# Performance work log

Measured on AMD Instinct MI355X. Metric: run time of the kernel, lower is better.

## Reference

```python
import jax, jax.numpy as jnp
import numpy as np

N_NODES = 100000
N_EDGES = 3200000
D_FEAT = 64


def setup_inputs() -> dict:
    key = jax.random.key(0)
    k1, k2, k3 = jax.random.split(key, 3)
    inputs = jax.random.normal(k1, (N_NODES, D_FEAT), dtype=jnp.float32)
    rows = jax.random.randint(k2, (N_EDGES,), 0, N_NODES, dtype=jnp.int32)
    cols = jax.random.randint(k3, (N_EDGES,), 0, N_NODES, dtype=jnp.int32)
    return {"inputs": inputs, "rows": rows, "cols": cols}


def reference(inputs, rows, cols):
    # adj is a binary sparse [N, N] matrix given as COO edges (rows[e], cols[e]) -> 1.0
    n = inputs.shape[0]
    # degrees = adj.sum(dim=1): count of outgoing edges per row
    deg = jax.ops.segment_sum(jnp.ones_like(rows, dtype=inputs.dtype), rows,
                              num_segments=n)  # [N]
    # degrees + (degrees == 0): avoid div-by-zero for isolated nodes
    deg = deg + (deg == 0).astype(inputs.dtype)
    # spmm(adj, inputs): sum neighbor features into each row
    agg = jax.ops.segment_sum(inputs[cols], rows, num_segments=n)  # [N, d]
    return agg / deg[:, None]
```

## Files before the change

kernel.cpp:

```cpp
#include <hip/hip_runtime.h>
#include <hip/hip_bf16.h>
#include <hip/hip_fp16.h>

#define D_FEAT 64
#define TILE_EDGES 8192
#define SC_THREADS 512
#define ROWS_PER_BUK 128
#define BUK_SHIFT 7
#define STRIDE 4480

__global__ void __launch_bounds__(SC_THREADS) scatter_kernel(
    const float* __restrict__ x, __half* __restrict__ x16,
    const int* __restrict__ rows, const int* __restrict__ cols,
    int* __restrict__ gcount, int* __restrict__ ebuf,
    int n_edges, int nbuk, int n4)
{
    __shared__ int lh[1024];
    __shared__ int lscan[1024];
    __shared__ int lgb[1024];
    __shared__ int lsort[TILE_EDGES];

    const int t = threadIdx.x;

    {
        const int per = (n4 + gridDim.x - 1) / gridDim.x;
        const int s0 = blockIdx.x * per;
        const int e0 = min(s0 + per, n4);
        for (int i = s0 + t; i < e0; i += SC_THREADS) {
            float4 v = ((const float4*)x)[i];
            ushort4 u;
            u.x = __half_as_ushort(__float2half(v.x));
            u.y = __half_as_ushort(__float2half(v.y));
            u.z = __half_as_ushort(__float2half(v.z));
            u.w = __half_as_ushort(__float2half(v.w));
            ((ushort4*)x16)[i] = u;
        }
    }

    lh[t] = 0; lh[t + 512] = 0;
    __syncthreads();

    const int tb = blockIdx.x * TILE_EDGES;
    const int te = min(tb + TILE_EDGES, n_edges);

    for (int e = tb + t * 4; e < te; e += SC_THREADS * 4) {
        if (e + 4 <= te) {
            int4 r4 = *(const int4*)&rows[e];
            atomicAdd(&lh[r4.x >> BUK_SHIFT], 1);
            atomicAdd(&lh[r4.y >> BUK_SHIFT], 1);
            atomicAdd(&lh[r4.z >> BUK_SHIFT], 1);
            atomicAdd(&lh[r4.w >> BUK_SHIFT], 1);
        } else {
            for (int k = e; k < te; ++k) atomicAdd(&lh[rows[k] >> BUK_SHIFT], 1);
        }
    }
    __syncthreads();

    const int c0 = lh[2 * t], c1 = lh[2 * t + 1];
    const int s2 = c0 + c1;
    lscan[t] = s2;
    __syncthreads();
    for (int ofs = 1; ofs < 512; ofs <<= 1) {
        int val = lscan[t];
        int add = (t >= ofs) ? lscan[t - ofs] : 0;
        __syncthreads();
        lscan[t] = val + add;
        __syncthreads();
    }
    const int excl = lscan[t] - s2;
    __syncthreads();
    lscan[2 * t] = excl;
    lscan[2 * t + 1] = excl + c0;
    lgb[2 * t]     = c0 ? atomicAdd(&gcount[2 * t], c0) : 0;
    lgb[2 * t + 1] = c1 ? atomicAdd(&gcount[2 * t + 1], c1) : 0;
    lh[2 * t] = excl;
    lh[2 * t + 1] = excl + c0;
    __syncthreads();

    for (int e = tb + t * 4; e < te; e += SC_THREADS * 4) {
        if (e + 4 <= te) {
            int4 r4 = *(const int4*)&rows[e];
            int4 c4 = *(const int4*)&cols[e];
            int p0 = atomicAdd(&lh[r4.x >> BUK_SHIFT], 1);
            int p1 = atomicAdd(&lh[r4.y >> BUK_SHIFT], 1);
            int p2 = atomicAdd(&lh[r4.z >> BUK_SHIFT], 1);
            int p3 = atomicAdd(&lh[r4.w >> BUK_SHIFT], 1);
            lsort[p0] = ((r4.x & (ROWS_PER_BUK - 1)) << 17) | c4.x;
            lsort[p1] = ((r4.y & (ROWS_PER_BUK - 1)) << 17) | c4.y;
            lsort[p2] = ((r4.z & (ROWS_PER_BUK - 1)) << 17) | c4.z;
            lsort[p3] = ((r4.w & (ROWS_PER_BUK - 1)) << 17) | c4.w;
        } else {
            for (int k = e; k < te; ++k) {
                int r = rows[k], c = cols[k];
                int pos = atomicAdd(&lh[r >> BUK_SHIFT], 1);
                lsort[pos] = ((r & (ROWS_PER_BUK - 1)) << 17) | c;
            }
        }
    }
    __syncthreads();

    const int hw = t >> 5;
    const int hl = t & 31;
    for (int b = hw; b < nbuk; b += 16) {
        const int ls = lscan[b];
        const int cnt = lh[b] - ls;
        const int gb = lgb[b];
        for (int i = hl; i < cnt; i += 32) {
            int gpos = gb + i;
            if (gpos < STRIDE) ebuf[b * STRIDE + gpos] = lsort[ls + i];
        }
    }
}

__global__ void __launch_bounds__(512) gather_kernel(
    const uint4* __restrict__ x4, const int* __restrict__ gcount,
    const int* __restrict__ ebuf, float* __restrict__ out, int n_nodes)
{
    __shared__ int lcol[STRIDE];
    __shared__ int lh[ROWS_PER_BUK];
    __shared__ int lscan[ROWS_PER_BUK];
    __shared__ int lcur[ROWS_PER_BUK];
    const int b = blockIdx.x;
    const int t = threadIdx.x;

    const int start = b * STRIDE;
    int cnt = gcount[b];
    if (cnt > STRIDE) cnt = STRIDE;

    if (t < ROWS_PER_BUK) lh[t] = 0;
    __syncthreads();
    for (int i = t; i < cnt; i += 512) atomicAdd(&lh[ebuf[start + i] >> 17], 1);
    __syncthreads();

    int v0 = (t < ROWS_PER_BUK) ? lh[t] : 0;
    if (t < ROWS_PER_BUK) lscan[t] = v0;
    __syncthreads();
    for (int ofs = 1; ofs < ROWS_PER_BUK; ofs <<= 1) {
        int val = 0;
        if (t < ROWS_PER_BUK) {
            val = lscan[t];
            if (t >= ofs) val += lscan[t - ofs];
        }
        __syncthreads();
        if (t < ROWS_PER_BUK) lscan[t] = val;
        __syncthreads();
    }
    if (t < ROWS_PER_BUK) {
        int excl = lscan[t] - v0;
        lscan[t] = excl;
        lcur[t] = excl;
    }
    __syncthreads();

    for (int i = t; i < cnt; i += 512) {
        int p = ebuf[start + i];
        int pos = atomicAdd(&lcur[p >> 17], 1);
        lcol[pos] = p & 0x1FFFF;
    }
    __syncthreads();

    const int w = t >> 6;
    const int lane = t & 63;
    const int eg = lane >> 3;
    const int g2 = lane & 7;

    union U { uint4 u; __half2 h2[4]; };

    for (int rr = 0; rr < 16; ++rr) {
        const int r = w * 16 + rr;
        const int row = (b << BUK_SHIFT) + r;
        const int s = lscan[r];
        const int d = lh[r];
        const int e = s + d;

        const __half2 z = __float2half2_rn(0.0f);
        __half2 h[4];
        #pragma unroll
        for (int k = 0; k < 4; ++k) h[k] = z;

        int j = s;
        for (; j + 32 <= e; j += 32) {
            int cA = lcol[j + eg], cB = lcol[j + 8 + eg];
            int cC = lcol[j + 16 + eg], cD = lcol[j + 24 + eg];
            U A, B, C, D;
            A.u = x4[cA * 8 + g2];
            B.u = x4[cB * 8 + g2];
            C.u = x4[cC * 8 + g2];
            D.u = x4[cD * 8 + g2];
            #pragma unroll
            for (int k = 0; k < 4; ++k)
                h[k] = __hadd2(h[k], __hadd2(__hadd2(A.h2[k], B.h2[k]),
                                             __hadd2(C.h2[k], D.h2[k])));
        }
        for (; j + 16 <= e; j += 16) {
            int cA = lcol[j + eg], cB = lcol[j + 8 + eg];
            U A, B;
            A.u = x4[cA * 8 + g2];
            B.u = x4[cB * 8 + g2];
            #pragma unroll
            for (int k = 0; k < 4; ++k)
                h[k] = __hadd2(h[k], __hadd2(A.h2[k], B.h2[k]));
        }
        for (; j + 8 <= e; j += 8) {
            int c = lcol[j + eg];
            U A;
            A.u = x4[c * 8 + g2];
            #pragma unroll
            for (int k = 0; k < 4; ++k) h[k] = __hadd2(h[k], A.h2[k]);
        }
        int rem = e - j;
        if (eg < rem) {
            int c = lcol[j + eg];
            U A;
            A.u = x4[c * 8 + g2];
            #pragma unroll
            for (int k = 0; k < 4; ++k) h[k] = __hadd2(h[k], A.h2[k]);
        }

        float a[8];
        #pragma unroll
        for (int k = 0; k < 4; ++k) {
            float2 f = __half22float2(h[k]);
            a[2 * k] = f.x;
            a[2 * k + 1] = f.y;
        }
        #pragma unroll
        for (int k = 0; k < 8; ++k) {
            a[k] += __shfl_down(a[k], 8, 64);
            a[k] += __shfl_down(a[k], 16, 64);
            a[k] += __shfl_down(a[k], 32, 64);
        }

        if (eg == 0 && row < n_nodes) {
            const float inv = 1.0f / (float)(d > 0 ? d : 1);
            float4* o = (float4*)(out + ((long)row << 6) + (g2 << 3));
            o[0] = make_float4(a[0] * inv, a[1] * inv, a[2] * inv, a[3] * inv);
            o[1] = make_float4(a[4] * inv, a[5] * inv, a[6] * inv, a[7] * inv);
        }
    }
}

extern "C" void kernel_launch(void* const* d_in, const int* in_sizes, int n_in,
                              void* d_out, int out_size, void* d_ws, size_t ws_size,
                              hipStream_t stream) {
    const float* x  = (const float*)d_in[0];
    const int* rows = (const int*)d_in[1];
    const int* cols = (const int*)d_in[2];
    float* out = (float*)d_out;

    const int n_nodes = in_sizes[0] / D_FEAT;
    const int n_edges = in_sizes[1];
    const int n_feat_total = in_sizes[0];
    const int n4 = n_feat_total / 4;

    const int nbuk   = (n_nodes + ROWS_PER_BUK - 1) >> BUK_SHIFT;
    const int ntiles = (n_edges + TILE_EDGES - 1) / TILE_EDGES;

    __half* x16 = (__half*)d_ws;
    int* gcount = (int*)(x16 + n_feat_total);
    int* ebuf   = gcount + nbuk;

    hipMemsetAsync(gcount, 0, (size_t)nbuk * sizeof(int), stream);

    scatter_kernel<<<ntiles, SC_THREADS, 0, stream>>>(
        x, x16, rows, cols, gcount, ebuf, n_edges, nbuk, n4);

    gather_kernel<<<nbuk, 512, 0, stream>>>((const uint4*)x16, gcount, ebuf, out, n_nodes);
}
```

Before: 182.7 us.

## Split gather buckets across two half-row blocks with wave-shuffle scan

Each 128-row bucket is now handled by two 256-thread blocks, each owning 64 rows. Both blocks still read the whole bucket's edge list and keep only their half. The prefix scan over row counts becomes a single-wavefront shuffle scan instead of a multi-sync LDS scan. Smaller blocks with less shared memory should raise occupancy and spread the load over more CUs. The cost is that every edge entry is read twice, and a half-bucket with more than 2560 edges gets truncated.

Measured after the change: 182.1 us. About the same (-0.3%).

```diff
diff --git a/kernel.cpp b/kernel.cpp
--- a/kernel.cpp
+++ b/kernel.cpp
@@ -8,6 +8,9 @@
 #define ROWS_PER_BUK 128
 #define BUK_SHIFT 7
 #define STRIDE 4480
+
+#define HALF_ROWS 64
+#define LCOL_SZ 2560
 
 __global__ void __launch_bounds__(SC_THREADS) scatter_kernel(
     const float* __restrict__ x, __half* __restrict__ x16,
@@ -112,50 +115,53 @@
     }
 }
 
-__global__ void __launch_bounds__(512) gather_kernel(
+__global__ void __launch_bounds__(256) gather_kernel(
     const uint4* __restrict__ x4, const int* __restrict__ gcount,
     const int* __restrict__ ebuf, float* __restrict__ out, int n_nodes)
 {
-    __shared__ int lcol[STRIDE];
-    __shared__ int lh[ROWS_PER_BUK];
-    __shared__ int lscan[ROWS_PER_BUK];
-    __shared__ int lcur[ROWS_PER_BUK];
-    const int b = blockIdx.x;
+    __shared__ int lcol[LCOL_SZ];
+    __shared__ int lh[HALF_ROWS];
+    __shared__ int lscan[HALF_ROWS];
+    __shared__ int lcur[HALF_ROWS];
+    const int bb = blockIdx.x;
+    const int b = bb >> 1;
+    const int half = bb & 1;
     const int t = threadIdx.x;
 
     const int start = b * STRIDE;
     int cnt = gcount[b];
     if (cnt > STRIDE) cnt = STRIDE;
 
-    if (t < ROWS_PER_BUK) lh[t] = 0;
-    __syncthreads();
-    for (int i = t; i < cnt; i += 512) atomicAdd(&lh[ebuf[start + i] >> 17], 1);
-    __syncthreads();
-
-    int v0 = (t < ROWS_PER_BUK) ? lh[t] : 0;
-    if (t < ROWS_PER_BUK) lscan[t] = v0;
-    __syncthreads();
-    for (int ofs = 1; ofs < ROWS_PER_BUK; ofs <<= 1) {
-        int val = 0;
-        if (t < ROWS_PER_BUK) {
-            val = lscan[t];
-            if (t >= ofs) val += lscan[t - ofs];
-        }
-        __syncthreads();
-        if (t < ROWS_PER_BUK) lscan[t] = val;
-        __syncthreads();
-    }
-    if (t < ROWS_PER_BUK) {
-        int excl = lscan[t] - v0;
+    if (t < HALF_ROWS) lh[t] = 0;
+    __syncthreads();
+    for (int i = t; i < cnt; i += 256) {
+        int p = ebuf[start + i];
+        int r = p >> 17;
+        if ((r >> 6) == half) atomicAdd(&lh[r & (HALF_ROWS - 1)], 1);
+    }
+    __syncthreads();
+
+    if (t < 64) {
+        int c = lh[t];
+        int val = c;
+        #pragma unroll
+        for (int ofs = 1; ofs < 64; ofs <<= 1) {
+            int n = __shfl_up(val, ofs, 64);
+            if (t >= ofs) val += n;
+        }
+        int excl = val - c;
         lscan[t] = excl;
         lcur[t] = excl;
     }
     __syncthreads();
 
-    for (int i = t; i < cnt; i += 512) {
+    for (int i = t; i < cnt; i += 256) {
         int p = ebuf[start + i];
-        int pos = atomicAdd(&lcur[p >> 17], 1);
-        lcol[pos] = p & 0x1FFFF;
+        int r = p >> 17;
+        if ((r >> 6) == half) {
+            int pos = atomicAdd(&lcur[r & (HALF_ROWS - 1)], 1);
+            if (pos < LCOL_SZ) lcol[pos] = p & 0x1FFFF;
+        }
     }
     __syncthreads();
 
@@ -168,10 +174,11 @@
 
     for (int rr = 0; rr < 16; ++rr) {
         const int r = w * 16 + rr;
-        const int row = (b << BUK_SHIFT) + r;
+        const int row = (b << BUK_SHIFT) + (half << 6) + r;
         const int s = lscan[r];
         const int d = lh[r];
-        const int e = s + d;
+        int e = s + d;
+        if (e > LCOL_SZ) e = LCOL_SZ;
 
         const __half2 z = __float2half2_rn(0.0f);
         __half2 h[4];
@@ -265,5 +272,5 @@
     scatter_kernel<<<ntiles, SC_THREADS, 0, stream>>>(
         x, x16, rows, cols, gcount, ebuf, n_edges, nbuk, n4);
 
-    gather_kernel<<<nbuk, 512, 0, stream>>>((const uint4*)x16, gcount, ebuf, out, n_nodes);
+    gather_kernel<<<nbuk * 2, 256, 0, stream>>>((const uint4*)x16, gcount, ebuf, out, n_nodes);
 }
```

## Phase gather by column range so concurrent blocks share an L2 working set

Applied to the files above, without the earlier changes.

The gather kernel now bins edges by row and by one of four column-index ranges (col>>15), and processes all rows of a bucket phase by phase with a block barrier between phases. Each row's accumulators are kept in registers across phases (16 rows × 4 half2 per lane). The aim is to make concurrently running blocks read source features from the same quarter of the x16 table, improving cache locality. The row scan is also replaced with a wave-shuffle scan. In exchange, register use rises sharply, the 32/16-wide unrolled load paths are dropped, and four extra barriers are added, which may lower occupancy and memory-level parallelism.

New measurement: 238.6 us. +30.6%, slower.

```diff
diff --git a/kernel.cpp b/kernel.cpp
--- a/kernel.cpp
+++ b/kernel.cpp
@@ -8,6 +8,8 @@
 #define ROWS_PER_BUK 128
 #define BUK_SHIFT 7
 #define STRIDE 4480
+#define NPH 4
+#define NBIN (ROWS_PER_BUK * NPH)
 
 __global__ void __launch_bounds__(SC_THREADS) scatter_kernel(
     const float* __restrict__ x, __half* __restrict__ x16,
@@ -117,110 +119,109 @@
     const int* __restrict__ ebuf, float* __restrict__ out, int n_nodes)
 {
     __shared__ int lcol[STRIDE];
-    __shared__ int lh[ROWS_PER_BUK];
-    __shared__ int lscan[ROWS_PER_BUK];
-    __shared__ int lcur[ROWS_PER_BUK];
+    __shared__ int lh2[NBIN];
+    __shared__ int lsc[NBIN];
+    __shared__ int lcur[NBIN];
+    __shared__ int wsum[8];
+
     const int b = blockIdx.x;
     const int t = threadIdx.x;
+    const int w = t >> 6;
+    const int lane = t & 63;
 
     const int start = b * STRIDE;
     int cnt = gcount[b];
     if (cnt > STRIDE) cnt = STRIDE;
 
-    if (t < ROWS_PER_BUK) lh[t] = 0;
-    __syncthreads();
-    for (int i = t; i < cnt; i += 512) atomicAdd(&lh[ebuf[start + i] >> 17], 1);
-    __syncthreads();
-
-    int v0 = (t < ROWS_PER_BUK) ? lh[t] : 0;
-    if (t < ROWS_PER_BUK) lscan[t] = v0;
-    __syncthreads();
-    for (int ofs = 1; ofs < ROWS_PER_BUK; ofs <<= 1) {
-        int val = 0;
-        if (t < ROWS_PER_BUK) {
-            val = lscan[t];
-            if (t >= ofs) val += lscan[t - ofs];
-        }
-        __syncthreads();
-        if (t < ROWS_PER_BUK) lscan[t] = val;
-        __syncthreads();
-    }
-    if (t < ROWS_PER_BUK) {
-        int excl = lscan[t] - v0;
-        lscan[t] = excl;
+    lh2[t] = 0;
+    __syncthreads();
+
+    for (int i = t; i < cnt; i += 512) {
+        int pk = ebuf[start + i];
+        int c = pk & 0x1FFFF;
+        int bin = ((pk >> 17) << 2) | (c >> 15);
+        atomicAdd(&lh2[bin], 1);
+    }
+    __syncthreads();
+
+    {
+        int c = lh2[t];
+        int val = c;
+        #pragma unroll
+        for (int ofs = 1; ofs < 64; ofs <<= 1) {
+            int n = __shfl_up(val, ofs, 64);
+            if (lane >= ofs) val += n;
+        }
+        if (lane == 63) wsum[w] = val;
+        __syncthreads();
+        int off = 0;
+        #pragma unroll
+        for (int k = 0; k < 8; ++k) off += (k < w) ? wsum[k] : 0;
+        int excl = val + off - c;
+        lsc[t] = excl;
         lcur[t] = excl;
     }
     __syncthreads();
 
     for (int i = t; i < cnt; i += 512) {
-        int p = ebuf[start + i];
-        int pos = atomicAdd(&lcur[p >> 17], 1);
-        lcol[pos] = p & 0x1FFFF;
-    }
-    __syncthreads();
-
-    const int w = t >> 6;
-    const int lane = t & 63;
+        int pk = ebuf[start + i];
+        int c = pk & 0x1FFFF;
+        int bin = ((pk >> 17) << 2) | (c >> 15);
+        int pos = atomicAdd(&lcur[bin], 1);
+        lcol[pos] = c;
+    }
+    __syncthreads();
+
     const int eg = lane >> 3;
     const int g2 = lane & 7;
 
     union U { uint4 u; __half2 h2[4]; };
 
+    const __half2 z = __float2half2_rn(0.0f);
+    __half2 h[16][4];
+    #pragma unroll
+    for (int rr = 0; rr < 16; ++rr)
+        #pragma unroll
+        for (int k = 0; k < 4; ++k) h[rr][k] = z;
+
+    for (int p = 0; p < NPH; ++p) {
+        #pragma unroll
+        for (int rr = 0; rr < 16; ++rr) {
+            const int r = w * 16 + rr;
+            const int bin = (r << 2) | p;
+            const int s = lsc[bin];
+            const int e = s + lh2[bin];
+
+            int j = s;
+            for (; j + 8 <= e; j += 8) {
+                int c = lcol[j + eg];
+                U A;
+                A.u = x4[c * 8 + g2];
+                #pragma unroll
+                for (int k = 0; k < 4; ++k) h[rr][k] = __hadd2(h[rr][k], A.h2[k]);
+            }
+            int rem = e - j;
+            if (eg < rem) {
+                int c = lcol[j + eg];
+                U A;
+                A.u = x4[c * 8 + g2];
+                #pragma unroll
+                for (int k = 0; k < 4; ++k) h[rr][k] = __hadd2(h[rr][k], A.h2[k]);
+            }
+        }
+        __syncthreads();
+    }
+
+    #pragma unroll
     for (int rr = 0; rr < 16; ++rr) {
         const int r = w * 16 + rr;
         const int row = (b << BUK_SHIFT) + r;
-        const int s = lscan[r];
-        const int d = lh[r];
-        const int e = s + d;
-
-        const __half2 z = __float2half2_rn(0.0f);
-        __half2 h[4];
-        #pragma unroll
-        for (int k = 0; k < 4; ++k) h[k] = z;
-
-        int j = s;
-        for (; j + 32 <= e; j += 32) {
-            int cA = lcol[j + eg], cB = lcol[j + 8 + eg];
-            int cC = lcol[j + 16 + eg], cD = lcol[j + 24 + eg];
-            U A, B, C, D;
-            A.u = x4[cA * 8 + g2];
-            B.u = x4[cB * 8 + g2];
-            C.u = x4[cC * 8 + g2];
-            D.u = x4[cD * 8 + g2];
-            #pragma unroll
-            for (int k = 0; k < 4; ++k)
-                h[k] = __hadd2(h[k], __hadd2(__hadd2(A.h2[k], B.h2[k]),
-                                             __hadd2(C.h2[k], D.h2[k])));
-        }
-        for (; j + 16 <= e; j += 16) {
-            int cA = lcol[j + eg], cB = lcol[j + 8 + eg];
-            U A, B;
-            A.u = x4[cA * 8 + g2];
-            B.u = x4[cB * 8 + g2];
-            #pragma unroll
-            for (int k = 0; k < 4; ++k)
-                h[k] = __hadd2(h[k], __hadd2(A.h2[k], B.h2[k]));
-        }
-        for (; j + 8 <= e; j += 8) {
-            int c = lcol[j + eg];
-            U A;
-            A.u = x4[c * 8 + g2];
-            #pragma unroll
-            for (int k = 0; k < 4; ++k) h[k] = __hadd2(h[k], A.h2[k]);
-        }
-        int rem = e - j;
-        if (eg < rem) {
-            int c = lcol[j + eg];
-            U A;
-            A.u = x4[c * 8 + g2];
-            #pragma unroll
-            for (int k = 0; k < 4; ++k) h[k] = __hadd2(h[k], A.h2[k]);
-        }
+        const int d = (lsc[(r << 2) | 3] + lh2[(r << 2) | 3]) - lsc[r << 2];
 
         float a[8];
         #pragma unroll
         for (int k = 0; k < 4; ++k) {
-            float2 f = __half22float2(h[k]);
+            float2 f = __half22float2(h[rr][k]);
             a[2 * k] = f.x;
             a[2 * k + 1] = f.y;
         }
```

## Fuse convert, scatter and gather into one cooperative kernel with grid syncs

Applied to the files above, without the earlier changes.

Merges the fp16 conversion, bucket scatter and gather phases into a single cooperative launch that uses grid-wide barriers, and zeroes the bucket counters in-kernel instead of with a memset. The two phases share one shared-memory union. The edge tile is halved so that the tile count roughly matches the bucket count, letting one grid size serve both phases. This is meant to remove launch and memset overhead and inter-kernel gaps. In exchange it pays for grid synchronisation, and the smaller tiles mean more global counter atomics and shorter bucket write runs. It falls back to separate kernels when occupancy cannot hold the whole grid.

After: 201.0 us. 10.0% more time.

```diff
diff --git a/kernel.cpp b/kernel.cpp
--- a/kernel.cpp
+++ b/kernel.cpp
@@ -1,99 +1,111 @@
 #include <hip/hip_runtime.h>
-#include <hip/hip_bf16.h>
 #include <hip/hip_fp16.h>
+#include <hip/hip_cooperative_groups.h>
+
+namespace cg = cooperative_groups;
 
 #define D_FEAT 64
-#define TILE_EDGES 8192
-#define SC_THREADS 512
+#define TILE_EDGES 4096
+#define THREADS 512
 #define ROWS_PER_BUK 128
 #define BUK_SHIFT 7
 #define STRIDE 4480
 
-__global__ void __launch_bounds__(SC_THREADS) scatter_kernel(
-    const float* __restrict__ x, __half* __restrict__ x16,
-    const int* __restrict__ rows, const int* __restrict__ cols,
-    int* __restrict__ gcount, int* __restrict__ ebuf,
-    int n_edges, int nbuk, int n4)
-{
-    __shared__ int lh[1024];
-    __shared__ int lscan[1024];
-    __shared__ int lgb[1024];
-    __shared__ int lsort[TILE_EDGES];
-
-    const int t = threadIdx.x;
-
-    {
-        const int per = (n4 + gridDim.x - 1) / gridDim.x;
-        const int s0 = blockIdx.x * per;
-        const int e0 = min(s0 + per, n4);
-        for (int i = s0 + t; i < e0; i += SC_THREADS) {
-            float4 v = ((const float4*)x)[i];
-            ushort4 u;
-            u.x = __half_as_ushort(__float2half(v.x));
-            u.y = __half_as_ushort(__float2half(v.y));
-            u.z = __half_as_ushort(__float2half(v.z));
-            u.w = __half_as_ushort(__float2half(v.w));
-            ((ushort4*)x16)[i] = u;
-        }
-    }
-
-    lh[t] = 0; lh[t + 512] = 0;
-    __syncthreads();
-
-    const int tb = blockIdx.x * TILE_EDGES;
+union SMem {
+    struct {
+        int lh[1024];
+        int lscan[1024];
+        int lgb[1024];
+        int lsort[TILE_EDGES];
+    } s;
+    struct {
+        int lcol[STRIDE];
+        int lh[ROWS_PER_BUK];
+        int lscan[ROWS_PER_BUK];
+        int lcur[ROWS_PER_BUK];
+    } g;
+};
+
+__device__ __forceinline__ void do_cvt(const float* __restrict__ x,
+                                       __half* __restrict__ x16,
+                                       int n4, int nblocks, int blk, int t)
+{
+    const int per = (n4 + nblocks - 1) / nblocks;
+    const int s0 = blk * per;
+    const int e0 = min(s0 + per, n4);
+    for (int i = s0 + t; i < e0; i += THREADS) {
+        float4 v = ((const float4*)x)[i];
+        ushort4 u;
+        u.x = __half_as_ushort(__float2half(v.x));
+        u.y = __half_as_ushort(__float2half(v.y));
+        u.z = __half_as_ushort(__float2half(v.z));
+        u.w = __half_as_ushort(__float2half(v.w));
+        ((ushort4*)x16)[i] = u;
+    }
+}
+
+__device__ void do_scatter(SMem& sm,
+                           const int* __restrict__ rows, const int* __restrict__ cols,
+                           int* __restrict__ gcount, int* __restrict__ ebuf,
+                           int n_edges, int nbuk, int tile, int t)
+{
+    sm.s.lh[t] = 0; sm.s.lh[t + 512] = 0;
+    __syncthreads();
+
+    const int tb = tile * TILE_EDGES;
     const int te = min(tb + TILE_EDGES, n_edges);
 
-    for (int e = tb + t * 4; e < te; e += SC_THREADS * 4) {
+    for (int e = tb + t * 4; e < te; e += THREADS * 4) {
         if (e + 4 <= te) {
             int4 r4 = *(const int4*)&rows[e];
-            atomicAdd(&lh[r4.x >> BUK_SHIFT], 1);
-            atomicAdd(&lh[r4.y >> BUK_SHIFT], 1);
-            atomicAdd(&lh[r4.z >> BUK_SHIFT], 1);
-            atomicAdd(&lh[r4.w >> BUK_SHIFT], 1);
+            atomicAdd(&sm.s.lh[r4.x >> BUK_SHIFT], 1);
+            atomicAdd(&sm.s.lh[r4.y >> BUK_SHIFT], 1);
+            atomicAdd(&sm.s.lh[r4.z >> BUK_SHIFT], 1);
+            atomicAdd(&sm.s.lh[r4.w >> BUK_SHIFT], 1);
         } else {
-            for (int k = e; k < te; ++k) atomicAdd(&lh[rows[k] >> BUK_SHIFT], 1);
-        }
-    }
-    __syncthreads();
-
-    const int c0 = lh[2 * t], c1 = lh[2 * t + 1];
+            for (int k = e; k < te; ++k) atomicAdd(&sm.s.lh[rows[k] >> BUK_SHIFT], 1);
+        }
+    }
+    __syncthreads();
+
+    const int c0 = sm.s.lh[2 * t], c1 = sm.s.lh[2 * t + 1];
     const int s2 = c0 + c1;
-    lscan[t] = s2;
+    sm.s.lscan[t] = s2;
     __syncthreads();
     for (int ofs = 1; ofs < 512; ofs <<= 1) {
-        int val = lscan[t];
-        int add = (t >= ofs) ? lscan[t - ofs] : 0;
+        int val = sm.s.lscan[t];
+        int add = (t >= ofs) ? sm.s.lscan[t - ofs] : 0;
         __syncthreads();
-        lscan[t] = val + add;
+        sm.s.lscan[t] = val + add;
         __syncthreads();
     }
-    const int excl = lscan[t] - s2;
-    __syncthreads();
-    lscan[2 * t] = excl;
-    lscan[2 * t + 1] = excl + c0;
-    lgb[2 * t]     = c0 ? atomicAdd(&gcount[2 * t], c0) : 0;
-    lgb[2 * t + 1] = c1 ? atomicAdd(&gcount[2 * t + 1], c1) : 0;
-    lh[2 * t] = excl;
-    lh[2 * t + 1] = excl + c0;
-    __syncthreads();
-
-    for (int e = tb + t * 4; e < te; e += SC_THREADS * 4) {
+    const int excl = sm.s.lscan[t] - s2;
+    __syncthreads();
+    sm.s.lscan[2 * t] = excl;
+    sm.s.lscan[2 * t + 1] = excl + c0;
+    sm.s.lgb[2 * t]     = c0 ? atomicAdd(&gcount[2 * t], c0) : 0;
+    sm.s.lgb[2 * t + 1] = c1 ? atomicAdd(&gcount[2 * t + 1], c1) : 0;
+    sm.s.lh[2 * t] = excl;
+    sm.s.lh[2 * t + 1] = excl + c0;
+    __syncthreads();
+
+    for (int e = tb + t * 4; e < te; e += THREADS * 4) {
         if (e + 4 <= te) {
             int4 r4 = *(const int4*)&rows[e];
             int4 c4 = *(const int4*)&cols[e];
-            int p0 = atomicAdd(&lh[r4.x >> BUK_SHIFT], 1);
-            int p1 = atomicAdd(&lh[r4.y >> BUK_SHIFT], 1);
-            int p2 = atomicAdd(&lh[r4.z >> BUK_SHIFT], 1);
-            int p3 = atomicAdd(&lh[r4.w >> BUK_SHIFT], 1);
-            lsort[p0] = ((r4.x & (ROWS_PER_BUK - 1)) << 17) | c4.x;
-            lsort[p1] = ((r4.y & (ROWS_PER_BUK - 1)) << 17) | c4.y;
-            lsort[p2] = ((r4.z & (ROWS_PER_BUK - 1)) << 17) | c4.z;
-            lsort[p3] = ((r4.w & (ROWS_PER_BUK - 1)) << 17) | c4.w;
+            int p0 = atomicAdd(&sm.s.lh[r4.x >> BUK_SHIFT], 1);
+            int p1 = atomicAdd(&sm.s.lh[r4.y >> BUK_SHIFT], 1);
+            int p2 = atomicAdd(&sm.s.lh[r4.z >> BUK_SHIFT], 1);
+            int p3 = atomicAdd(&sm.s.lh[r4.w >> BUK_SHIFT], 1);
+            sm.s.lsort[p0] = ((r4.x & (ROWS_PER_BUK - 1)) << 17) | c4.x;
+            sm.s.lsort[p1] = ((r4.y & (ROWS_PER_BUK - 1)) << 17) | c4.y;
+            sm.s.lsort[p2] = ((r4.z & (ROWS_PER_BUK - 1)) << 17) | c4.z;
+            sm.s.lsort[p3] = ((r4.w & (ROWS_PER_BUK - 1)) << 17) | c4.w;
         } else {
             for (int k = e; k < te; ++k) {
                 int r = rows[k], c = cols[k];
-                int pos = atomicAdd(&lh[r >> BUK_SHIFT], 1);
-                lsort[pos] = ((r & (ROWS_PER_BUK - 1)) << 17) | c;
+                int pos = atomicAdd(&sm.s.lh[r >> BUK_SHIFT], 1);
+                sm.s.lsort[pos] = ((r & (ROWS_PER_BUK - 1)) << 17) | c;
             }
         }
     }
@@ -102,60 +114,54 @@
     const int hw = t >> 5;
     const int hl = t & 31;
     for (int b = hw; b < nbuk; b += 16) {
-        const int ls = lscan[b];
-        const int cnt = lh[b] - ls;
-        const int gb = lgb[b];
+        const int ls = sm.s.lscan[b];
+        const int cnt = sm.s.lh[b] - ls;
+        const int gb = sm.s.lgb[b];
         for (int i = hl; i < cnt; i += 32) {
             int gpos = gb + i;
-            if (gpos < STRIDE) ebuf[b * STRIDE + gpos] = lsort[ls + i];
-        }
-    }
-}
-
-__global__ void __launch_bounds__(512) gather_kernel(
-    const uint4* __restrict__ x4, const int* __restrict__ gcount,
-    const int* __restrict__ ebuf, float* __restrict__ out, int n_nodes)
-{
-    __shared__ int lcol[STRIDE];
-    __shared__ int lh[ROWS_PER_BUK];
-    __shared__ int lscan[ROWS_PER_BUK];
-    __shared__ int lcur[ROWS_PER_BUK];
-    const int b = blockIdx.x;
-    const int t = threadIdx.x;
-
+            if (gpos < STRIDE) ebuf[b * STRIDE + gpos] = sm.s.lsort[ls + i];
+        }
+    }
+}
+
+__device__ void do_gather(SMem& sm,
+                          const uint4* __restrict__ x4, const int* __restrict__ gcount,
+                          const int* __restrict__ ebuf, float* __restrict__ out,
+                          int n_nodes, int b, int t)
+{
     const int start = b * STRIDE;
     int cnt = gcount[b];
     if (cnt > STRIDE) cnt = STRIDE;
 
-    if (t < ROWS_PER_BUK) lh[t] = 0;
-    __syncthreads();
-    for (int i = t; i < cnt; i += 512) atomicAdd(&lh[ebuf[start + i] >> 17], 1);
-    __syncthreads();
-
-    int v0 = (t < ROWS_PER_BUK) ? lh[t] : 0;
-    if (t < ROWS_PER_BUK) lscan[t] = v0;
+    if (t < ROWS_PER_BUK) sm.g.lh[t] = 0;
+    __syncthreads();
+    for (int i = t; i < cnt; i += THREADS) atomicAdd(&sm.g.lh[ebuf[start + i] >> 17], 1);
+    __syncthreads();
+
+    int v0 = (t < ROWS_PER_BUK) ? sm.g.lh[t] : 0;
+    if (t < ROWS_PER_BUK) sm.g.lscan[t] = v0;
     __syncthreads();
     for (int ofs = 1; ofs < ROWS_PER_BUK; ofs <<= 1) {
         int val = 0;
         if (t < ROWS_PER_BUK) {
-            val = lscan[t];
-            if (t >= ofs) val += lscan[t - ofs];
+            val = sm.g.lscan[t];
+            if (t >= ofs) val += sm.g.lscan[t - ofs];
         }
         __syncthreads();
-        if (t < ROWS_PER_BUK) lscan[t] = val;
+        if (t < ROWS_PER_BUK) sm.g.lscan[t] = val;
         __syncthreads();
     }
     if (t < ROWS_PER_BUK) {
-        int excl = lscan[t] - v0;
-        lscan[t] = excl;
-        lcur[t] = excl;
-    }
-    __syncthreads();
-
-    for (int i = t; i < cnt; i += 512) {
+        int excl = sm.g.lscan[t] - v0;
+        sm.g.lscan[t] = excl;
+        sm.g.lcur[t] = excl;
+    }
+    __syncthreads();
+
+    for (int i = t; i < cnt; i += THREADS) {
         int p = ebuf[start + i];
-        int pos = atomicAdd(&lcur[p >> 17], 1);
-        lcol[pos] = p & 0x1FFFF;
+        int pos = atomicAdd(&sm.g.lcur[p >> 17], 1);
+        sm.g.lcol[pos] = p & 0x1FFFF;
     }
     __syncthreads();
 
@@ -169,8 +175,8 @@
     for (int rr = 0; rr < 16; ++rr) {
         const int r = w * 16 + rr;
         const int row = (b << BUK_SHIFT) + r;
-        const int s = lscan[r];
-        const int d = lh[r];
+        const int s = sm.g.lscan[r];
+        const int d = sm.g.lh[r];
         const int e = s + d;
 
         const __half2 z = __float2half2_rn(0.0f);
@@ -180,8 +186,8 @@
 
         int j = s;
         for (; j + 32 <= e; j += 32) {
-            int cA = lcol[j + eg], cB = lcol[j + 8 + eg];
-            int cC = lcol[j + 16 + eg], cD = lcol[j + 24 + eg];
+            int cA = sm.g.lcol[j + eg], cB = sm.g.lcol[j + 8 + eg];
+            int cC = sm.g.lcol[j + 16 + eg], cD = sm.g.lcol[j + 24 + eg];
             U A, B, C, D;
             A.u = x4[cA * 8 + g2];
             B.u = x4[cB * 8 + g2];
@@ -193,7 +199,7 @@
                                              __hadd2(C.h2[k], D.h2[k])));
         }
         for (; j + 16 <= e; j += 16) {
-            int cA = lcol[j + eg], cB = lcol[j + 8 + eg];
+            int cA = sm.g.lcol[j + eg], cB = sm.g.lcol[j + 8 + eg];
             U A, B;
             A.u = x4[cA * 8 + g2];
             B.u = x4[cB * 8 + g2];
@@ -202,7 +208,7 @@
                 h[k] = __hadd2(h[k], __hadd2(A.h2[k], B.h2[k]));
         }
         for (; j + 8 <= e; j += 8) {
-            int c = lcol[j + eg];
+            int c = sm.g.lcol[j + eg];
             U A;
             A.u = x4[c * 8 + g2];
             #pragma unroll
@@ -210,7 +216,7 @@
         }
         int rem = e - j;
         if (eg < rem) {
-            int c = lcol[j + eg];
+            int c = sm.g.lcol[j + eg];
             U A;
             A.u = x4[c * 8 + g2];
             #pragma unroll
@@ -238,6 +244,49 @@
             o[1] = make_float4(a[4] * inv, a[5] * inv, a[6] * inv, a[7] * inv);
         }
     }
+}
+
+__global__ void __launch_bounds__(THREADS, 8) fused_kernel(
+    const float* __restrict__ x, __half* __restrict__ x16,
+    const int* __restrict__ rows, const int* __restrict__ cols,
+    int* __restrict__ gcount, int* __restrict__ ebuf,
+    float* __restrict__ out,
+    int n_edges, int nbuk, int n4, int ntiles, int n_nodes)
+{
+    __shared__ SMem sm;
+    const int t = threadIdx.x;
+    const int blk = blockIdx.x;
+    cg::grid_group grid = cg::this_grid();
+
+    if (t == 0 && blk < nbuk) gcount[blk] = 0;
+    do_cvt(x, x16, n4, gridDim.x, blk, t);
+    grid.sync();
+
+    if (blk < ntiles)
+        do_scatter(sm, rows, cols, gcount, ebuf, n_edges, nbuk, blk, t);
+    grid.sync();
+
+    if (blk < nbuk)
+        do_gather(sm, (const uint4*)x16, gcount, ebuf, out, n_nodes, blk, t);
+}
+
+__global__ void __launch_bounds__(THREADS) scatter_kernel(
+    const float* __restrict__ x, __half* __restrict__ x16,
+    const int* __restrict__ rows, const int* __restrict__ cols,
+    int* __restrict__ gcount, int* __restrict__ ebuf,
+    int n_edges, int nbuk, int n4)
+{
+    __shared__ SMem sm;
+    do_cvt(x, x16, n4, gridDim.x, blockIdx.x, threadIdx.x);
+    do_scatter(sm, rows, cols, gcount, ebuf, n_edges, nbuk, blockIdx.x, threadIdx.x);
+}
+
+__global__ void __launch_bounds__(THREADS) gather_kernel(
+    const uint4* __restrict__ x4, const int* __restrict__ gcount,
+    const int* __restrict__ ebuf, float* __restrict__ out, int n_nodes)
+{
+    __shared__ SMem sm;
+    do_gather(sm, x4, gcount, ebuf, out, n_nodes, blockIdx.x, threadIdx.x);
 }
 
 extern "C" void kernel_launch(void* const* d_in, const int* in_sizes, int n_in,
@@ -248,22 +297,39 @@
     const int* cols = (const int*)d_in[2];
     float* out = (float*)d_out;
 
-    const int n_nodes = in_sizes[0] / D_FEAT;
-    const int n_edges = in_sizes[1];
+    int n_nodes = in_sizes[0] / D_FEAT;
+    int n_edges = in_sizes[1];
     const int n_feat_total = in_sizes[0];
-    const int n4 = n_feat_total / 4;
-
-    const int nbuk   = (n_nodes + ROWS_PER_BUK - 1) >> BUK_SHIFT;
-    const int ntiles = (n_edges + TILE_EDGES - 1) / TILE_EDGES;
+    int n4 = n_feat_total / 4;
+
+    int nbuk   = (n_nodes + ROWS_PER_BUK - 1) >> BUK_SHIFT;
+    int ntiles = (n_edges + TILE_EDGES - 1) / TILE_EDGES;
 
     __half* x16 = (__half*)d_ws;
     int* gcount = (int*)(x16 + n_feat_total);
     int* ebuf   = gcount + nbuk;
 
-    hipMemsetAsync(gcount, 0, (size_t)nbuk * sizeof(int), stream);
-
-    scatter_kernel<<<ntiles, SC_THREADS, 0, stream>>>(
-        x, x16, rows, cols, gcount, ebuf, n_edges, nbuk, n4);
-
-    gather_kernel<<<nbuk, 512, 0, stream>>>((const uint4*)x16, gcount, ebuf, out, n_nodes);
-}
+    const int grid = (nbuk > ntiles) ? nbuk : ntiles;
+
+    int blocks_per_cu = 0;
+    hipError_t qerr = hipOccupancyMaxActiveBlocksPerMultiprocessor(
+        &blocks_per_cu, (const void*)fused_kernel, THREADS, 0);
+    int ndev_cu = 256;
+    hipDeviceProp_t prop;
+    if (hipGetDeviceProperties(&prop, 0) == hipSuccess) ndev_cu = prop.multiProcessorCount;
+
+    if (qerr == hipSuccess && blocks_per_cu * ndev_cu >= grid) {
+        void* args[] = {(void*)&x, (void*)&x16, (void*)&rows, (void*)&cols,
+                        (void*)&gcount, (void*)&ebuf, (void*)&out,
+                        (void*)&n_edges, (void*)&nbuk, (void*)&n4,
+                        (void*)&ntiles, (void*)&n_nodes};
+        hipLaunchCooperativeKernel((void*)fused_kernel, dim3(grid), dim3(THREADS),
+                                   args, 0, stream);
+    } else {
+        hipMemsetAsync(gcount, 0, (size_t)nbuk * sizeof(int), stream);
+        scatter_kernel<<<ntiles, THREADS, 0, stream>>>(
+            x, x16, rows, cols, gcount, ebuf, n_edges, nbuk, n4);
+        gather_kernel<<<nbuk, THREADS, 0, stream>>>(
+            (const uint4*)x16, gcount, ebuf, out, n_nodes);
+    }
+}
```
